# Kernel tuning notes

Measured on AMD Instinct MI355X. Metric: run time of the kernel, lower is better.

Reference implementation:

```python
import jax, jax.numpy as jnp
import numpy as np

EPS = 1e-5  # BatchNorm1d default eps


def gcn_conv(x, row, col, w, n):
    # symmetric normalized aggregation: out[c] = sum_e d[row]^-1/2 d[col]^-1/2 w_e x[row]
    deg = jax.ops.segment_sum(w, col, num_segments=n)           # weighted in-degree [N]
    dinv = jnp.where(deg > 0, jax.lax.rsqrt(deg), 0.0)          # nan_to_num guard
    norm = dinv[row] * dinv[col] * w                            # [E]
    msg = x[row] * norm[:, None]                                # [E, H] gather
    return jax.ops.segment_sum(msg, col, num_segments=n)        # [N, H] scatter-add


def batchnorm(x):
    # BatchNorm1d(affine=False, track_running_stats=False): batch stats, biased var
    mu = jnp.mean(x, axis=0)
    var = jnp.mean((x - mu) ** 2, axis=0)
    return (x - mu) * jax.lax.rsqrt(var + EPS)


def setup_inputs() -> dict:
    key = jax.random.key(0)
    ks = jax.random.split(key, 7)
    N, E, D, H = 100000, 1600000, 128, 128
    x = jax.random.normal(ks[0], (N, D), dtype=jnp.float32)
    edge_index = jax.random.randint(ks[1], (2, E), 0, N, dtype=jnp.int32)
    edge_weight = jax.random.uniform(ks[2], (E,), dtype=jnp.float32)
    # xavier_uniform gain=1: limit = sqrt(6/(fan_in+fan_out))
    lim0 = float(np.sqrt(6.0 / (D + H)))
    lim1 = float(np.sqrt(6.0 / (H + H)))
    W0 = jax.random.uniform(ks[3], (H, D), dtype=jnp.float32, minval=-lim0, maxval=lim0)
    W1 = jax.random.uniform(ks[4], (H, H), dtype=jnp.float32, minval=-lim1, maxval=lim1)
    b0 = jnp.zeros((H,), jnp.float32)
    b1 = jnp.zeros((H,), jnp.float32)
    return {"x": x, "edge_index": edge_index, "edge_weight": edge_weight,
            "W0": W0, "b0": b0, "W1": W1, "b1": b1}


def reference(x, edge_index, edge_weight, W0, b0, W1, b1):
    n = x.shape[0]
    row, col = edge_index[0], edge_index[1]
    # layer 0: linear -> gcn_conv -> bias -> batchnorm -> relu
    h = x @ W0.T
    h = gcn_conv(h, row, col, edge_weight, n)
    h = jax.nn.relu(batchnorm(h + b0))
    # final layer: linear -> gcn_conv -> bias
    h = h @ W1.T
    h = gcn_conv(h, row, col, edge_weight, n)
    return h + b1
```

## Files before the change

kernel.cpp:

```cpp
#include <hip/hip_runtime.h>
#include <cstdint>
#include <cstddef>

#define EPSF 1e-5f
#define BKT 256
#define BKT_SHIFT 8
#define SC_E 4096

typedef unsigned long long ull;
typedef __attribute__((ext_vector_type(8))) short bf16x8;
typedef __attribute__((ext_vector_type(4))) float f32x4;


__global__ __launch_bounds__(512) void bucket_hist(const int* __restrict__ col,
                                                   int* __restrict__ bhist, int E, int NB) {
    __shared__ int lh[512];
    const int t = threadIdx.x;
    lh[t] = 0;
    __syncthreads();
    for (int e = blockIdx.x * 512 + t; e < E; e += gridDim.x * 512)
        atomicAdd(&lh[col[e] >> BKT_SHIFT], 1);
    __syncthreads();
    if (t < NB && lh[t]) atomicAdd(&bhist[t], lh[t]);
}

__global__ __launch_bounds__(512) void scan_buckets(const int* __restrict__ bhist,
                                                    int* __restrict__ bstart,
                                                    int* __restrict__ bcursor,
                                                    int* __restrict__ rs,
                                                    int NB, int N, int E) {
    __shared__ int part[512];
    const int t = threadIdx.x;
    part[t] = (t < NB) ? bhist[t] : 0;
    __syncthreads();
    for (int off = 1; off < 512; off <<= 1) {
        int v = (t >= off) ? part[t - off] : 0;
        __syncthreads();
        part[t] += v;
        __syncthreads();
    }
    int excl = (t == 0) ? 0 : part[t - 1];
    if (t < NB) { bstart[t] = excl; bcursor[t] = excl; }
    if (t == 0) { bstart[NB] = E; rs[N] = E; }
}

__global__ __launch_bounds__(512) void bucket_scatter(const int* __restrict__ row,
                                                      const int* __restrict__ col,
                                                      const float* __restrict__ w,
                                                      int* __restrict__ bcursor,
                                                      int2* __restrict__ brecs,
                                                      int E, int NB) {
    __shared__ int lh[512], lstart[512], lcur[512], gbase[512];
    __shared__ int   sm[SC_E];
    __shared__ float sw[SC_E];
    __shared__ short sb[SC_E];

    const int t = threadIdx.x;
    const int base = blockIdx.x * SC_E;
    const int cnt = min(SC_E, E - base);

    lh[t] = 0;
    __syncthreads();

    int   myb[8], mym[8];
    float myw[8];
#pragma unroll
    for (int k = 0; k < 8; ++k) {
        int i = t + k * 512;
        if (i < cnt) {
            int e = base + i;
            int r = row[e], c = col[e];
            myb[k] = c >> BKT_SHIFT;
            mym[k] = ((c & (BKT - 1)) << 17) | r;
            myw[k] = w[e];
            atomicAdd(&lh[myb[k]], 1);
        } else myb[k] = -1;
    }
    __syncthreads();

    int v = lh[t];
    lstart[t] = v;
    __syncthreads();
    for (int off = 1; off < 512; off <<= 1) {
        int u = (t >= off) ? lstart[t - off] : 0;
        __syncthreads();
        lstart[t] += u;
        __syncthreads();
    }
    int excl = lstart[t] - v;
    __syncthreads();
    lstart[t] = excl;
    lcur[t]   = excl;
    gbase[t]  = (t < NB) ? atomicAdd(&bcursor[t], v) : 0;
    __syncthreads();

#pragma unroll
    for (int k = 0; k < 8; ++k) {
        if (myb[k] >= 0) {
            int slot = atomicAdd(&lcur[myb[k]], 1);
            sm[slot] = mym[k];
            sw[slot] = myw[k];
            sb[slot] = (short)myb[k];
        }
    }
    __syncthreads();

    for (int j = t; j < cnt; j += 512) {
        int b = sb[j];
        int pos = gbase[b] + (j - lstart[b]);
        brecs[pos] = make_int2(sm[j], __float_as_int(sw[j]));
    }
}

__global__ __launch_bounds__(256) void bucket_build_p1(const int2* __restrict__ brecs,
                                                       const int* __restrict__ bstart,
                                                       int* __restrict__ rs,
                                                       float* __restrict__ dinv, int N) {
    __shared__ int   lcnt[256], lscan[256];
    __shared__ float ldeg[256];
    const int b = blockIdx.x, t = threadIdx.x;
    const int s = bstart[b], e = bstart[b + 1];
    const int node0 = b << BKT_SHIFT;
    const int nNodes = min(BKT, N - node0);

    lcnt[t] = 0;
    ldeg[t] = 0.f;
    __syncthreads();

    for (int i = s + t; i < e; i += 256) {
        int2 r = brecs[i];
        int cl = r.x >> 17;
        atomicAdd(&lcnt[cl], 1);
        atomicAdd(&ldeg[cl], __int_as_float(r.y));
    }
    __syncthreads();

    int v = lcnt[t];
    lscan[t] = v;
    __syncthreads();
    for (int off = 1; off < 256; off <<= 1) {
        int u = (t >= off) ? lscan[t - off] : 0;
        __syncthreads();
        lscan[t] += u;
        __syncthreads();
    }
    if (t < nNodes) {
        rs[node0 + t] = s + (lscan[t] - v);
        float d = ldeg[t];
        dinv[node0 + t] = (d > 0.f) ? rsqrtf(d) : 0.f;
    }
}

__global__ __launch_bounds__(256) void bucket_place(const int2* __restrict__ brecs,
                                                    const int* __restrict__ bstart,
                                                    const int* __restrict__ rs,
                                                    const float* __restrict__ dinv,
                                                    int2* __restrict__ sedge, int N) {
    __shared__ int   lcur[256];
    __shared__ float ld[256];
    const int b = blockIdx.x, t = threadIdx.x;
    const int s = bstart[b], e = bstart[b + 1];
    const int node0 = b << BKT_SHIFT;
    const int nNodes = min(BKT, N - node0);

    lcur[t] = (t < nNodes) ? rs[node0 + t] : 0;
    ld[t]   = (t < nNodes) ? dinv[node0 + t] : 0.f;
    __syncthreads();

    for (int i = s + t; i < e; i += 256) {
        int2 r = brecs[i];
        int cl   = r.x >> 17;
        int rowi = r.x & 0x1FFFF;
        float nrm = dinv[rowi] * ld[cl] * __int_as_float(r.y);
        int slot = atomicAdd(&lcur[cl], 1);
        sedge[slot] = make_int2(rowi, __float_as_int(nrm));
    }
}

__device__ __forceinline__ ushort f2bf(float f) {
    uint b = __float_as_uint(f);
    return (ushort)((b + 0x7FFFu + ((b >> 16) & 1u)) >> 16);
}
__device__ __forceinline__ float bf2f(ushort u) {
    return __uint_as_float((uint)u << 16);
}
__device__ __forceinline__ uint4 pack8(const float* f) {
    uint4 o;
    o.x = f2bf(f[0]) | ((uint)f2bf(f[1]) << 16);
    o.y = f2bf(f[2]) | ((uint)f2bf(f[3]) << 16);
    o.z = f2bf(f[4]) | ((uint)f2bf(f[5]) << 16);
    o.w = f2bf(f[6]) | ((uint)f2bf(f[7]) << 16);
    return o;
}

template <int MODE>
__global__ __launch_bounds__(256) void gemm128_mfma(const void* __restrict__ Xv,
                                                    const float* __restrict__ W,
                                                    ushort* __restrict__ Y, int N,
                                                    const float* __restrict__ sums,
                                                    float invN) {
    __shared__ __align__(16) ushort Alds[64][128];
    __shared__ __align__(16) ushort Blds[128][128];
    __shared__ float bnmu[128], bnrs[128];

    const int t = threadIdx.x;

    if constexpr (MODE == 2) {
        if (t < 128) {
            float mu  = sums[t] * invN;
            float var = sums[128 + t] * invN - mu * mu;
            bnmu[t] = mu;
            bnrs[t] = rsqrtf(var + EPSF);
        }
    }

    for (int i = t; i < 128 * 16; i += 256) {
        int j = i >> 4, kc = (i & 15) << 3;
        float f[8];
        *(float4*)&f[0] = *(const float4*)&W[j * 128 + kc];
        *(float4*)&f[4] = *(const float4*)&W[j * 128 + kc + 4];
        *(uint4*)&Blds[j][kc ^ ((j & 7) << 3)] = pack8(f);
    }

    const int lane  = t & 63;
    const int wv    = t >> 6;
    const int arow  = wv * 16 + (lane & 15);
    const int klane = (lane >> 4) << 3;
    const int cq    = lane & 15;
    const int nTiles = (N + 63) >> 6;

    for (int tile = blockIdx.x; tile < nTiles; tile += gridDim.x) {
        const int n0 = tile * 64;
        __syncthreads();

        for (int i = t; i < 64 * 16; i += 256) {
            int r = i >> 4, kc = (i & 15) << 3;
            int n = n0 + r;
            uint4 v = make_uint4(0u, 0u, 0u, 0u);
            if (n < N) {
                if constexpr (MODE == 0) {
                    float f[8];
                    *(float4*)&f[0] = *(const float4*)&((const float*)Xv)[(size_t)n * 128 + kc];
                    *(float4*)&f[4] = *(const float4*)&((const float*)Xv)[(size_t)n * 128 + kc + 4];
                    v = pack8(f);
                } else {
                    uint4 raw = *(const uint4*)&((const ushort*)Xv)[(size_t)n * 128 + kc];
                    const uint* rw = &raw.x;
                    float f[8];
#pragma unroll
                    for (int k = 0; k < 4; ++k) {
                        float lo = __uint_as_float(rw[k] << 16);
                        float hi = __uint_as_float(rw[k] & 0xFFFF0000u);
                        f[2 * k]     = fmaxf((lo - bnmu[kc + 2 * k])     * bnrs[kc + 2 * k],     0.f);
                        f[2 * k + 1] = fmaxf((hi - bnmu[kc + 2 * k + 1]) * bnrs[kc + 2 * k + 1], 0.f);
                    }
                    v = pack8(f);
                }
            }
            *(uint4*)&Alds[r][kc ^ ((r & 7) << 3)] = v;
        }
        __syncthreads();

        f32x4 acc[8] = {};
        for (int ks = 0; ks < 4; ++ks) {
            const int k0 = ks * 32 + klane;
            bf16x8 a = *(const bf16x8*)&Alds[arow][k0 ^ ((arow & 7) << 3)];
#pragma unroll
            for (int tl = 0; tl < 8; ++tl) {
                int colr = tl * 16 + cq;
                bf16x8 bb = *(const bf16x8*)&Blds[colr][k0 ^ ((colr & 7) << 3)];
                acc[tl] = __builtin_amdgcn_mfma_f32_16x16x32_bf16(a, bb, acc[tl], 0, 0, 0);
            }
        }

        const int r0 = n0 + wv * 16 + ((lane >> 4) << 2);
#pragma unroll
        for (int tl = 0; tl < 8; ++tl) {
#pragma unroll
            for (int reg = 0; reg < 4; ++reg) {
                int rr = r0 + reg;
                if (rr < N) Y[(size_t)rr * 128 + tl * 16 + cq] = f2bf(acc[tl][reg]);
            }
        }
    }
}

__device__ __forceinline__ float bflo(uint v) { return __uint_as_float(v << 16); }
__device__ __forceinline__ float bfhi(uint v) { return __uint_as_float(v & 0xFFFF0000u); }

template <bool OUT_BF16>
__global__ __launch_bounds__(256) void agg_gather(const ushort* __restrict__ Hin,
                                                  const int2* __restrict__ sedge,
                                                  const int* __restrict__ rs,
                                                  const float* __restrict__ bias,
                                                  void* __restrict__ Hout, int N, int E) {
    int c = blockIdx.x * 4 + (threadIdx.x >> 6);
    if (c >= N) return;
    const int lane = threadIdx.x & 63;
    const int g  = lane >> 4;
    const int lq = lane & 15;

    float acc[8] = {0.f, 0.f, 0.f, 0.f, 0.f, 0.f, 0.f, 0.f};
    if (bias && g == 0) {
        *(float4*)&acc[0] = *(const float4*)&bias[lq * 8];
        *(float4*)&acc[4] = *(const float4*)&bias[lq * 8 + 4];
    }

    const int e0 = rs[c];
    const int deg = rs[c + 1] - e0;

    for (int base = 0; base < deg; base += 64) {
        int m = min(64, deg - base);
        int idx = e0 + base + lane;
        int2 rec = sedge[idx < E ? idx : E - 1];

        int j = 0;
#define QLOAD(p, rr, ww, vv)                                                    \
        int   rr = __shfl(rec.x, j + 4 * (p) + g);                              \
        float ww = __int_as_float(__shfl(rec.y, j + 4 * (p) + g));              \
        uint4 vv = *(const uint4*)&Hin[(size_t)rr * 128 + lq * 8];
#define QACC(ww, vv)                                                            \
        acc[0] = fmaf(ww, bflo(vv.x), acc[0]); acc[1] = fmaf(ww, bfhi(vv.x), acc[1]); \
        acc[2] = fmaf(ww, bflo(vv.y), acc[2]); acc[3] = fmaf(ww, bfhi(vv.y), acc[3]); \
        acc[4] = fmaf(ww, bflo(vv.z), acc[4]); acc[5] = fmaf(ww, bfhi(vv.z), acc[5]); \
        acc[6] = fmaf(ww, bflo(vv.w), acc[6]); acc[7] = fmaf(ww, bfhi(vv.w), acc[7]);

        for (; j + 15 < m; j += 16) {
            QLOAD(0, r0, w0, v0) QLOAD(1, r1, w1, v1)
            QLOAD(2, r2, w2, v2) QLOAD(3, r3, w3, v3)
            QACC(w0, v0) QACC(w1, v1) QACC(w2, v2) QACC(w3, v3)
        }
        for (; j < m; j += 4) {
            int jj = j + g;
            int sl = (jj < m) ? jj : j;
            int   r0 = __shfl(rec.x, sl);
            float w0 = __int_as_float(__shfl(rec.y, sl));
            if (jj >= m) w0 = 0.f;
            uint4 v0 = *(const uint4*)&Hin[(size_t)r0 * 128 + lq * 8];
            QACC(w0, v0)
        }
#undef QLOAD
#undef QACC
    }

#pragma unroll
    for (int k = 0; k < 8; ++k) {
        acc[k] += __shfl_xor(acc[k], 16);
        acc[k] += __shfl_xor(acc[k], 32);
    }

    if (g == 0) {
        if constexpr (OUT_BF16) {
            uint4 o;
            o.x = f2bf(acc[0]) | ((uint)f2bf(acc[1]) << 16);
            o.y = f2bf(acc[2]) | ((uint)f2bf(acc[3]) << 16);
            o.z = f2bf(acc[4]) | ((uint)f2bf(acc[5]) << 16);
            o.w = f2bf(acc[6]) | ((uint)f2bf(acc[7]) << 16);
            *(uint4*)&((uint*)Hout)[(size_t)c * 64 + lq * 4] = o;
        } else {
            *(float4*)&((float*)Hout)[(size_t)c * 128 + lq * 8]     = *(float4*)&acc[0];
            *(float4*)&((float*)Hout)[(size_t)c * 128 + lq * 8 + 4] = *(float4*)&acc[4];
        }
    }
}

__global__ __launch_bounds__(256) void bn_stats(const ushort* __restrict__ H,
                                                float* __restrict__ sums, int N) {
    int j = threadIdx.x & 127;
    float s = 0.f, s2 = 0.f;
    for (int n = blockIdx.x * 2 + (threadIdx.x >> 7); n < N; n += gridDim.x * 2) {
        float v = bf2f(H[(size_t)n * 128 + j]);
        s += v; s2 += v * v;
    }
    atomicAdd(&sums[j], s);
    atomicAdd(&sums[128 + j], s2);
}

extern "C" void kernel_launch(void* const* d_in, const int* in_sizes, int n_in,
                              void* d_out, int out_size, void* d_ws, size_t ws_size,
                              hipStream_t stream) {
    const float* x  = (const float*)d_in[0];
    const int*   ei = (const int*)d_in[1];
    const float* ew = (const float*)d_in[2];
    const float* W0 = (const float*)d_in[3];
    const float* W1 = (const float*)d_in[5];
    const float* b1 = (const float*)d_in[6];

    const int N = in_sizes[0] / 128;
    const int E = in_sizes[2];
    const int* row = ei;
    const int* col = ei + E;
    const int NB = (N + BKT - 1) >> BKT_SHIFT;

    uintptr_t base = (uintptr_t)d_ws;
    auto alloc = [&](size_t bytes) {
        uintptr_t p = base;
        base += (bytes + 255) & ~(size_t)255;
        return (void*)p;
    };
    float*  dinv   = (float*) alloc((size_t)N * 4);
    float*  sums   = (float*) alloc(256 * 4);
    int*    bhist  = (int*)   alloc((size_t)(NB + 1) * 4);
    int*    bstart = (int*)   alloc((size_t)(NB + 1) * 4);
    int*    bcursor= (int*)   alloc((size_t)NB * 4);
    int*    rs     = (int*)   alloc((size_t)(N + 1) * 4);
    int2*   sedge  = (int2*)  alloc((size_t)E * 8);
    ushort* hA     = (ushort*)alloc((size_t)N * 128 * 2);
    ushort* hB     = (ushort*)alloc((size_t)N * 128 * 2);
    int2*   brecs  = (int2*)hB;
    float*  out    = (float*) d_out;
    (void)ws_size; (void)n_in; (void)out_size;

    const float invN = 1.f / (float)N;

    hipMemsetAsync(bhist, 0, (size_t)(NB + 1) * 4, stream);
    hipMemsetAsync(sums, 0, 256 * 4, stream);

    bucket_hist<<<1024, 512, 0, stream>>>(col, bhist, E, NB);
    scan_buckets<<<1, 512, 0, stream>>>(bhist, bstart, bcursor, rs, NB, N, E);
    bucket_scatter<<<(E + SC_E - 1) / SC_E, 512, 0, stream>>>(row, col, ew, bcursor,
                                                              brecs, E, NB);
    bucket_build_p1<<<NB, 256, 0, stream>>>(brecs, bstart, rs, dinv, N);
    bucket_place<<<NB, 256, 0, stream>>>(brecs, bstart, rs, dinv, sedge, N);

    const int nTiles = (N + 63) / 64;
    const int gemmGrid = nTiles < 512 ? nTiles : 512;

    gemm128_mfma<0><<<gemmGrid, 256, 0, stream>>>(x, W0, hA, N, nullptr, 0.f);

    agg_gather<true><<<(N + 3) / 4, 256, 0, stream>>>(hA, sedge, rs, nullptr, hB, N, E);

    bn_stats<<<512, 256, 0, stream>>>(hB, sums, N);

    gemm128_mfma<2><<<gemmGrid, 256, 0, stream>>>(hB, W1, hA, N, sums, invN);

    agg_gather<false><<<(N + 3) / 4, 256, 0, stream>>>(hA, sedge, rs, b1, out, N, E);
}
```

Before: 291.8 us.

## Factor GCN normalization into GEMM epilogue and split aggregation across XCD halves

The symmetric normalization is factored: the source-side dinv now scales rows in the GEMM epilogue, and the destination-side dinv is applied once per node after aggregation. This lets the two CSR build kernels merge into one that stores raw edge weights, which removes the random dinv[row] gather per edge. The aggregation kernel also splits each node's 128 features into two 64-feature halves handled by different blocks, mapped by block-id bits so each XCD group touches only half of the feature rows, aiming to improve L2 locality. The cost is twice as many gather blocks, each doing half-width loads, plus some extra index arithmetic.

Result: slower. 357.4 us (+22.5%).

```diff
diff --git a/kernel.cpp b/kernel.cpp
--- a/kernel.cpp
+++ b/kernel.cpp
@@ -112,11 +112,12 @@
     }
 }
 
-__global__ __launch_bounds__(256) void bucket_build_p1(const int2* __restrict__ brecs,
-                                                       const int* __restrict__ bstart,
-                                                       int* __restrict__ rs,
-                                                       float* __restrict__ dinv, int N) {
-    __shared__ int   lcnt[256], lscan[256];
+__global__ __launch_bounds__(256) void bucket_build(const int2* __restrict__ brecs,
+                                                    const int* __restrict__ bstart,
+                                                    int* __restrict__ rs,
+                                                    float* __restrict__ dinv,
+                                                    int2* __restrict__ sedge, int N) {
+    __shared__ int   lcnt[256], lscan[256], lcur[256];
     __shared__ float ldeg[256];
     const int b = blockIdx.x, t = threadIdx.x;
     const int s = bstart[b], e = bstart[b + 1];
@@ -144,36 +145,19 @@
         lscan[t] += u;
         __syncthreads();
     }
+    int excl = lscan[t] - v;
+    lcur[t] = s + excl;
     if (t < nNodes) {
-        rs[node0 + t] = s + (lscan[t] - v);
+        rs[node0 + t] = s + excl;
         float d = ldeg[t];
         dinv[node0 + t] = (d > 0.f) ? rsqrtf(d) : 0.f;
     }
-}
-
-__global__ __launch_bounds__(256) void bucket_place(const int2* __restrict__ brecs,
-                                                    const int* __restrict__ bstart,
-                                                    const int* __restrict__ rs,
-                                                    const float* __restrict__ dinv,
-                                                    int2* __restrict__ sedge, int N) {
-    __shared__ int   lcur[256];
-    __shared__ float ld[256];
-    const int b = blockIdx.x, t = threadIdx.x;
-    const int s = bstart[b], e = bstart[b + 1];
-    const int node0 = b << BKT_SHIFT;
-    const int nNodes = min(BKT, N - node0);
-
-    lcur[t] = (t < nNodes) ? rs[node0 + t] : 0;
-    ld[t]   = (t < nNodes) ? dinv[node0 + t] : 0.f;
     __syncthreads();
 
     for (int i = s + t; i < e; i += 256) {
         int2 r = brecs[i];
-        int cl   = r.x >> 17;
-        int rowi = r.x & 0x1FFFF;
-        float nrm = dinv[rowi] * ld[cl] * __int_as_float(r.y);
-        int slot = atomicAdd(&lcur[cl], 1);
-        sedge[slot] = make_int2(rowi, __float_as_int(nrm));
+        int slot = atomicAdd(&lcur[r.x >> 17], 1);
+        sedge[slot] = make_int2(r.x & 0x1FFFF, r.y);
     }
 }
 
@@ -198,7 +182,8 @@
                                                     const float* __restrict__ W,
                                                     ushort* __restrict__ Y, int N,
                                                     const float* __restrict__ sums,
-                                                    float invN) {
+                                                    float invN,
+                                                    const float* __restrict__ dinv) {
     __shared__ __align__(16) ushort Alds[64][128];
     __shared__ __align__(16) ushort Blds[128][128];
     __shared__ float bnmu[128], bnrs[128];
@@ -274,12 +259,16 @@
         }
 
         const int r0 = n0 + wv * 16 + ((lane >> 4) << 2);
+        float dv[4];
+#pragma unroll
+        for (int reg = 0; reg < 4; ++reg)
+            dv[reg] = (r0 + reg < N) ? dinv[r0 + reg] : 0.f;
 #pragma unroll
         for (int tl = 0; tl < 8; ++tl) {
 #pragma unroll
             for (int reg = 0; reg < 4; ++reg) {
                 int rr = r0 + reg;
-                if (rr < N) Y[(size_t)rr * 128 + tl * 16 + cq] = f2bf(acc[tl][reg]);
+                if (rr < N) Y[(size_t)rr * 128 + tl * 16 + cq] = f2bf(acc[tl][reg] * dv[reg]);
             }
         }
     }
@@ -292,19 +281,24 @@
 __global__ __launch_bounds__(256) void agg_gather(const ushort* __restrict__ Hin,
                                                   const int2* __restrict__ sedge,
                                                   const int* __restrict__ rs,
+                                                  const float* __restrict__ dinv,
                                                   const float* __restrict__ bias,
-                                                  void* __restrict__ Hout, int N, int E) {
-    int c = blockIdx.x * 4 + (threadIdx.x >> 6);
+                                                  void* __restrict__ Hout,
+                                                  int N, int E, int G) {
+    const int bid  = blockIdx.x;
+    const int xcd  = bid & 7;
+    const int half = xcd >> 2;
+    const int ng   = (bid >> 3) * 4 + (xcd & 3);
+    if (ng >= G) return;
+    const int c = ng * 4 + (threadIdx.x >> 6);
     if (c >= N) return;
+
     const int lane = threadIdx.x & 63;
     const int g  = lane >> 4;
     const int lq = lane & 15;
-
-    float acc[8] = {0.f, 0.f, 0.f, 0.f, 0.f, 0.f, 0.f, 0.f};
-    if (bias && g == 0) {
-        *(float4*)&acc[0] = *(const float4*)&bias[lq * 8];
-        *(float4*)&acc[4] = *(const float4*)&bias[lq * 8 + 4];
-    }
+    const int fb = half * 64 + lq * 4;
+
+    float acc[4] = {0.f, 0.f, 0.f, 0.f};
 
     const int e0 = rs[c];
     const int deg = rs[c + 1] - e0;
@@ -318,12 +312,10 @@
 #define QLOAD(p, rr, ww, vv)                                                    \
         int   rr = __shfl(rec.x, j + 4 * (p) + g);                              \
         float ww = __int_as_float(__shfl(rec.y, j + 4 * (p) + g));              \
-        uint4 vv = *(const uint4*)&Hin[(size_t)rr * 128 + lq * 8];
+        uint2 vv = *(const uint2*)&Hin[(size_t)rr * 128 + fb];
 #define QACC(ww, vv)                                                            \
         acc[0] = fmaf(ww, bflo(vv.x), acc[0]); acc[1] = fmaf(ww, bfhi(vv.x), acc[1]); \
-        acc[2] = fmaf(ww, bflo(vv.y), acc[2]); acc[3] = fmaf(ww, bfhi(vv.y), acc[3]); \
-        acc[4] = fmaf(ww, bflo(vv.z), acc[4]); acc[5] = fmaf(ww, bfhi(vv.z), acc[5]); \
-        acc[6] = fmaf(ww, bflo(vv.w), acc[6]); acc[7] = fmaf(ww, bfhi(vv.w), acc[7]);
+        acc[2] = fmaf(ww, bflo(vv.y), acc[2]); acc[3] = fmaf(ww, bfhi(vv.y), acc[3]);
 
         for (; j + 15 < m; j += 16) {
             QLOAD(0, r0, w0, v0) QLOAD(1, r1, w1, v1)
@@ -336,7 +328,7 @@
             int   r0 = __shfl(rec.x, sl);
             float w0 = __int_as_float(__shfl(rec.y, sl));
             if (jj >= m) w0 = 0.f;
-            uint4 v0 = *(const uint4*)&Hin[(size_t)r0 * 128 + lq * 8];
+            uint2 v0 = *(const uint2*)&Hin[(size_t)r0 * 128 + fb];
             QACC(w0, v0)
         }
 #undef QLOAD
@@ -344,22 +336,27 @@
     }
 
 #pragma unroll
-    for (int k = 0; k < 8; ++k) {
+    for (int k = 0; k < 4; ++k) {
         acc[k] += __shfl_xor(acc[k], 16);
         acc[k] += __shfl_xor(acc[k], 32);
     }
 
     if (g == 0) {
+        const float dc = dinv[c];
+        float val[4];
+#pragma unroll
+        for (int k = 0; k < 4; ++k) val[k] = acc[k] * dc;
+        if (bias) {
+            float4 bv = *(const float4*)&bias[fb];
+            val[0] += bv.x; val[1] += bv.y; val[2] += bv.z; val[3] += bv.w;
+        }
         if constexpr (OUT_BF16) {
-            uint4 o;
-            o.x = f2bf(acc[0]) | ((uint)f2bf(acc[1]) << 16);
-            o.y = f2bf(acc[2]) | ((uint)f2bf(acc[3]) << 16);
-            o.z = f2bf(acc[4]) | ((uint)f2bf(acc[5]) << 16);
-            o.w = f2bf(acc[6]) | ((uint)f2bf(acc[7]) << 16);
-            *(uint4*)&((uint*)Hout)[(size_t)c * 64 + lq * 4] = o;
+            uint2 o;
+            o.x = f2bf(val[0]) | ((uint)f2bf(val[1]) << 16);
+            o.y = f2bf(val[2]) | ((uint)f2bf(val[3]) << 16);
+            *(uint2*)&((uint*)Hout)[(size_t)c * 64 + half * 32 + lq * 2] = o;
         } else {
-            *(float4*)&((float*)Hout)[(size_t)c * 128 + lq * 8]     = *(float4*)&acc[0];
-            *(float4*)&((float*)Hout)[(size_t)c * 128 + lq * 8 + 4] = *(float4*)&acc[4];
+            *(float4*)&((float*)Hout)[(size_t)c * 128 + fb] = *(float4*)val;
         }
     }
 }
@@ -420,19 +417,22 @@
     scan_buckets<<<1, 512, 0, stream>>>(bhist, bstart, bcursor, rs, NB, N, E);
     bucket_scatter<<<(E + SC_E - 1) / SC_E, 512, 0, stream>>>(row, col, ew, bcursor,
                                                               brecs, E, NB);
-    bucket_build_p1<<<NB, 256, 0, stream>>>(brecs, bstart, rs, dinv, N);
-    bucket_place<<<NB, 256, 0, stream>>>(brecs, bstart, rs, dinv, sedge, N);
+    bucket_build<<<NB, 256, 0, stream>>>(brecs, bstart, rs, dinv, sedge, N);
 
     const int nTiles = (N + 63) / 64;
     const int gemmGrid = nTiles < 512 ? nTiles : 512;
-
-    gemm128_mfma<0><<<gemmGrid, 256, 0, stream>>>(x, W0, hA, N, nullptr, 0.f);
-
-    agg_gather<true><<<(N + 3) / 4, 256, 0, stream>>>(hA, sedge, rs, nullptr, hB, N, E);
+    const int G = (N + 3) / 4;
+    const int convGrid = 8 * ((G + 3) / 4);
+
+    gemm128_mfma<0><<<gemmGrid, 256, 0, stream>>>(x, W0, hA, N, nullptr, 0.f, dinv);
+
+    agg_gather<true><<<convGrid, 256, 0, stream>>>(hA, sedge, rs, dinv, nullptr,
+                                                   hB, N, E, G);
 
     bn_stats<<<512, 256, 0, stream>>>(hB, sums, N);
 
-    gemm128_mfma<2><<<gemmGrid, 256, 0, stream>>>(hB, W1, hA, N, sums, invN);
-
-    agg_gather<false><<<(N + 3) / 4, 256, 0, stream>>>(hA, sedge, rs, b1, out, N, E);
-}
+    gemm128_mfma<2><<<gemmGrid, 256, 0, stream>>>(hB, W1, hA, N, sums, invN, dinv);
+
+    agg_gather<false><<<convGrid, 256, 0, stream>>>(hA, sedge, rs, dinv, b1,
+                                                    out, N, E, G);
+}
```
